# Kernel optimization log

Measured on AMD Instinct MI355X. Metric: run time of the kernel, lower is better.

Reference implementation:

```python
import jax, jax.numpy as jnp
import numpy as np

B, HEAD, IMG, STRIDE, C = 8, 512, 1280, 32, 20
FMP = IMG // STRIDE            # 40
N = FMP * FMP                  # 1600 grid cells
CONF_T, NMS_T = 0.001, 0.6


def setup_inputs() -> dict:
    key = jax.random.key(0)
    ks = jax.random.split(key, 8)
    s3 = 1.0 / np.sqrt(HEAD * 9)   # fan-in scaled 3x3 weights
    s1 = 1.0 / np.sqrt(HEAD)
    return {
        "x": jax.random.normal(ks[0], (B, HEAD, FMP, FMP), jnp.float32),
        "cls_w": jax.random.normal(ks[1], (2, HEAD, HEAD, 3, 3), jnp.float32) * s3,
        "cls_b": jnp.zeros((2, HEAD), jnp.float32),
        "reg_w": jax.random.normal(ks[2], (4, HEAD, HEAD, 3, 3), jnp.float32) * s3,
        "reg_b": jnp.zeros((4, HEAD), jnp.float32),
        "obj_w": jax.random.normal(ks[3], (1, HEAD, 1, 1), jnp.float32) * s1,
        "obj_b": jnp.zeros((1,), jnp.float32),
        "clsp_w": jax.random.normal(ks[4], (C, HEAD, 1, 1), jnp.float32) * s1,
        "clsp_b": jnp.zeros((C,), jnp.float32),
        "regp_w": jax.random.normal(ks[5], (4, HEAD, 1, 1), jnp.float32) * s1,
        "regp_b": jnp.zeros((4,), jnp.float32),
    }


def _conv(x, w, b, pad):
    y = jax.lax.conv_general_dilated(
        x, w, (1, 1), [(pad, pad), (pad, pad)],
        dimension_numbers=("NCHW", "OIHW", "NCHW"))
    return y + b[None, :, None, None]


def _leaky(v):
    return jnp.where(v > 0, v, 0.1 * v)


def _head(x, cls_w, cls_b, reg_w, reg_b, obj_w, obj_b, clsp_w, clsp_b, regp_w, regp_b):
    cf = x
    for i in range(2):
        cf = _leaky(_conv(cf, cls_w[i], cls_b[i], 1))
    rf = x
    for i in range(4):
        rf = _leaky(_conv(rf, reg_w[i], reg_b[i], 1))
    b = x.shape[0]
    obj = _conv(rf, obj_w, obj_b, 0).reshape(b, 1, N).transpose(0, 2, 1)   # [B,N,1]
    cls = _conv(cf, clsp_w, clsp_b, 0).reshape(b, C, N).transpose(0, 2, 1) # [B,N,C]
    reg = _conv(rf, regp_w, regp_b, 0).reshape(b, 4, N).transpose(0, 2, 1) # [B,N,4]
    # decode_bbox (center_sample=False)
    gy, gx = jnp.meshgrid(jnp.arange(FMP), jnp.arange(FMP), indexing="ij")
    grid = jnp.stack([gx, gy], -1).reshape(N, 2).astype(jnp.float32)       # [N,2]
    xy = jax.nn.sigmoid(reg[..., :2]) + grid
    wh = jnp.exp(reg[..., 2:])
    box = jnp.concatenate([xy - wh * 0.5, xy + wh * 0.5], -1) * STRIDE     # [B,N,4]
    bboxes = jnp.clip(box / IMG, 0.0, 1.0)
    scores = jax.nn.sigmoid(obj) * jax.nn.softmax(cls, axis=-1)            # [B,N,C]
    return bboxes, scores


def _nms_mask(iou, scores, mask):
    # greedy NMS over boxes where mask is True; returns bool keep mask [N]
    order = jnp.argsort(-jnp.where(mask, scores, -jnp.inf))
    rank = jnp.argsort(order)  # rank[j] = position of box j in score order
    def body(i, keep):
        idx = order[i]
        sup = (iou[idx] > NMS_T) & keep[idx] & (rank > i)
        return keep & ~sup
    return jax.lax.fori_loop(0, scores.shape[0], body, mask)


def _post_one(boxes, scores):
    # boxes [N,4], scores [N,C] -> per-image postprocess
    cls_inds = jnp.argmax(scores, axis=1)
    best = jnp.take_along_axis(scores, cls_inds[:, None], axis=1)[:, 0]
    conf = best >= CONF_T
    x1, y1, x2, y2 = boxes[:, 0], boxes[:, 1], boxes[:, 2], boxes[:, 3]
    areas = (x2 - x1) * (y2 - y1)
    xx1 = jnp.maximum(x1[:, None], x1[None, :])
    yy1 = jnp.maximum(y1[:, None], y1[None, :])
    xx2 = jnp.minimum(x2[:, None], x2[None, :])
    yy2 = jnp.minimum(y2[:, None], y2[None, :])
    w = jnp.maximum(1e-28, xx2 - xx1)
    h = jnp.maximum(1e-28, yy2 - yy1)
    inter = w * h
    iou = inter / (areas[:, None] + areas[None, :] - inter + 1e-14)  # [N,N]
    keep_c = jax.vmap(
        lambda c: _nms_mask(iou, best, conf & (cls_inds == c)))(jnp.arange(C))
    return best, cls_inds.astype(jnp.int32), keep_c.any(0)


def reference(x, cls_w, cls_b, reg_w, reg_b, obj_w, obj_b,
              clsp_w, clsp_b, regp_w, regp_b):
    bboxes, scores = _head(x, cls_w, cls_b, reg_w, reg_b,
                           obj_w, obj_b, clsp_w, clsp_b, regp_w, regp_b)
    best, cls_inds, keep = jax.vmap(_post_one)(bboxes, scores)
    # fixed-shape outputs: boxes [B,N,4], best score [B,N], class id [B,N], keep mask [B,N]
    return bboxes, best, cls_inds, keep
```

## Files before the change

### kernel.cpp

```cpp
#include <hip/hip_runtime.h>
#include <math.h>

#define CH    512
#define FMPX  40
#define PW    42
#define PADN  1764
#define NP    1600
#define BATCH 8
#define NCLS  20
#define CONF_THR 0.001f
#define NMS_THR  0.6f

typedef _Float16 v8h __attribute__((ext_vector_type(8)));
typedef float    v4f __attribute__((ext_vector_type(4)));

#define FPLANE  ((size_t)BATCH * PADN * CH)
#define WSZ     ((size_t)9 * CH * CH)

__device__ __forceinline__ int padidx(int p) { return p + 2 * (p / FMPX) + PW + 1; }

typedef __attribute__((address_space(1))) const void* gas_t;
typedef __attribute__((address_space(3))) void*       las_t;
__device__ __forceinline__ void gl2lds16(const void* g, void* l) {
    __builtin_amdgcn_global_load_lds((gas_t)g, (las_t)l, 16, 0, 0);
}
__device__ __forceinline__ unsigned lds_addr(void* p) {
    return (unsigned)(uintptr_t)(las_t)p;
}
__device__ __forceinline__ v8h lds_b128(unsigned a) {
    v8h r;
    asm volatile("ds_read_b128 %0, %1" : "=v"(r) : "v"(a));
    return r;
}

__global__ __launch_bounds__(256)
void border_zero(uint4* __restrict__ ws) {
    int idx = blockIdx.x * 256 + threadIdx.x;
    int u    = idx & 63;
    int cell = (idx >> 6) % 164;
    int b    = (idx / (64 * 164)) & 7;
    int pl   = idx / (64 * 164 * 8);
    int pi;
    if (cell < 42)      pi = cell;
    else if (cell < 84) pi = 41 * PW + (cell - 42);
    else { int r = cell - 84; pi = (1 + (r >> 1)) * PW + ((r & 1) ? 41 : 0); }
    size_t hoff = (size_t)pl * FPLANE + (size_t)b * (PADN * CH) + (size_t)pi * CH;
    ws[(hoff >> 3) + u] = make_uint4(0u, 0u, 0u, 0u);
}

__global__ __launch_bounds__(256)
void xprep_kernel(const float* __restrict__ x, _Float16* __restrict__ Xh,
                  _Float16* __restrict__ Xl) {
    __shared__ float T[64][65];
    const int t = threadIdx.x;
    const int p0  = blockIdx.x * 64;
    const int ci0 = blockIdx.y * 64;
    const int b   = blockIdx.z;
#pragma unroll
    for (int it = 0; it < 16; ++it) {
        int row = (t >> 6) + 4 * it;
        int col = t & 63;
        T[col][row] = x[((size_t)b * CH + ci0 + row) * NP + p0 + col];
    }
    __syncthreads();
#pragma unroll
    for (int it = 0; it < 16; ++it) {
        int posl = (t >> 6) + 4 * it;
        int ci   = t & 63;
        float v = T[posl][ci];
        _Float16 h = (_Float16)v;
        _Float16 l = (_Float16)((v - (float)h) * 2048.0f);
        size_t o = (size_t)b * (PADN * CH) + (size_t)padidx(p0 + posl) * CH + ci0 + ci;
        Xh[o] = h; Xl[o] = l;
    }
}

__global__ __launch_bounds__(256)
void wtrans_kernel(const float* __restrict__ w, _Float16* __restrict__ Wh,
                   _Float16* __restrict__ Wl) {
    __shared__ float tile[32][289];
    const int t = threadIdx.x;
    const int co0 = blockIdx.x * 32;
    const int ci0 = blockIdx.y * 32;
#pragma unroll
    for (int g = 0; g < 36; ++g) {
        int l = t + 256 * g;
        int co = l / 288, j = l - co * 288;
        tile[co][j] = w[(size_t)(co0 + co) * 4608 + ci0 * 9 + j];
    }
    __syncthreads();
#pragma unroll
    for (int tap = 0; tap < 9; ++tap) {
#pragma unroll
        for (int cg = 0; cg < 4; ++cg) {
            int co = cg * 8 + (t >> 5);
            int ci = t & 31;
            float v = tile[co][ci * 9 + tap];
            _Float16 h = (_Float16)(16.0f * v);
            _Float16 l = (_Float16)((v - (float)h * 0.0625f) * 32768.0f);
            size_t o = ((size_t)tap * CH + co0 + co) * CH + ci0 + ci;
            Wh[o] = h; Wl[o] = l;
        }
    }
}

__global__ __launch_bounds__(512, 2)
void conv_dual(const _Float16* __restrict__ I0h, const _Float16* __restrict__ I0l,
               const _Float16* __restrict__ W0h, const _Float16* __restrict__ W0l,
               const float* __restrict__ bias0,
               _Float16* __restrict__ O0h, _Float16* __restrict__ O0l,
               const _Float16* __restrict__ I1h, const _Float16* __restrict__ I1l,
               const _Float16* __restrict__ W1h, const _Float16* __restrict__ W1l,
               const float* __restrict__ bias1,
               _Float16* __restrict__ O1h, _Float16* __restrict__ O1l) {
    __shared__ _Float16 sm[73728];
    const int t = threadIdx.x;
    const int w = t >> 6, l = t & 63;
    const int quad = l >> 4, col = l & 15;
    const int ph = w >> 2, cq = w & 3;

    const int bid = blockIdx.x;
    const int b   = bid & 7;
    const int q   = bid >> 3;
    const int cid = q / 26;
    const int r   = q - 26 * cid;
    const int co0 = (r & 1) * 256;
    const int p0  = (r >> 1) * 128;

    const _Float16* Ih = cid ? I1h : I0h;
    const _Float16* Il = cid ? I1l : I0l;
    const _Float16* Wh = cid ? W1h : W0h;
    const _Float16* Wl = cid ? W1l : W0l;
    const float*  bias = cid ? bias1 : bias0;
    _Float16* Oh = cid ? O1h : O0h;
    _Float16* Ol = cid ? O1l : O0l;

    const size_t boff = (size_t)b * (PADN * CH);

    const size_t sA  = boff + (size_t)padidx(p0 + 16 * w + col) * CH + quad * 8;
    const size_t sB0 = (size_t)(co0 + 32 * w + col) * CH + quad * 8;
    const int dA = w * 512 + l * 8;
    const int dB = 8192 + (2 * w) * 512 + l * 8;

    const unsigned smB = lds_addr(sm);
    unsigned aRh[4], aRl[4], bRh[4], bRl[4];
#pragma unroll
    for (int i = 0; i < 4; ++i) {
        aRh[i] = smB + (ph * 4 + i) * 1024 + l * 16;
        aRl[i] = aRh[i] + 8192;
    }
#pragma unroll
    for (int j = 0; j < 4; ++j) {
        bRh[j] = smB + 16384 + (cq * 4 + j) * 1024 + l * 16;
        bRl[j] = bRh[j] + 16384;
    }

    auto stage_chunk = [&](int mm, unsigned nH) {
        const int tap = mm >> 4, cc = (mm & 15) << 5;
        const int ty  = tap / 3;
        const int tsh = ((ty - 1) * PW + (tap - ty * 3 - 1)) * CH + cc;
        const size_t wo = (size_t)tap * (CH * CH) + cc;
        gl2lds16(Ih + sA + tsh,           sm + nH + dA);
        gl2lds16(Il + sA + tsh,           sm + nH + 4096 + dA);
        gl2lds16(Wh + wo + sB0,           sm + nH + dB);
        gl2lds16(Wh + wo + sB0 + 16 * CH, sm + nH + dB + 512);
        gl2lds16(Wl + wo + sB0,           sm + nH + 8192 + dB);
        gl2lds16(Wl + wo + sB0 + 16 * CH, sm + nH + 8192 + dB + 512);
    };

    v4f acc1[4][4], acc2[4][4];
#pragma unroll
    for (int i = 0; i < 4; ++i)
#pragma unroll
        for (int j = 0; j < 4; ++j) {
            acc1[i][j] = (v4f){0.f, 0.f, 0.f, 0.f};
            acc2[i][j] = (v4f){0.f, 0.f, 0.f, 0.f};
        }

    stage_chunk(0, 0);
    stage_chunk(1, 24576);
    asm volatile("s_waitcnt vmcnt(6)" ::: "memory");
    __builtin_amdgcn_s_barrier();

    unsigned c0H = 0, c1H = 24576, c2H = 49152;

#pragma unroll 1
    for (int m = 0; m < 144; ++m) {
        const unsigned bufB = c0H * 2;

        v8h ah[4], al[4], bh[4], bl[4];
#pragma unroll
        for (int i = 0; i < 4; ++i) {
            ah[i] = lds_b128(aRh[i] + bufB);
            al[i] = lds_b128(aRl[i] + bufB);
        }
        bh[0] = lds_b128(bRh[0] + bufB);
        bl[0] = lds_b128(bRl[0] + bufB);

        if (m < 142) stage_chunk(m + 2, c2H);

#pragma unroll
        for (int j = 0; j < 4; ++j) {
            if (j < 3) {
                bh[j + 1] = lds_b128(bRh[j + 1] + bufB);
                bl[j + 1] = lds_b128(bRl[j + 1] + bufB);
                asm volatile("s_waitcnt lgkmcnt(2)" ::: "memory");
            } else {
                asm volatile("s_waitcnt lgkmcnt(0)" ::: "memory");
            }
            __builtin_amdgcn_sched_barrier(0);
            __builtin_amdgcn_s_setprio(1);
#pragma unroll
            for (int i = 0; i < 4; ++i)
                acc1[i][j] = __builtin_amdgcn_mfma_f32_16x16x32_f16(ah[i], bh[j], acc1[i][j], 0, 0, 0);
#pragma unroll
            for (int i = 0; i < 4; ++i)
                acc2[i][j] = __builtin_amdgcn_mfma_f32_16x16x32_f16(ah[i], bl[j], acc2[i][j], 0, 0, 0);
#pragma unroll
            for (int i = 0; i < 4; ++i)
                acc2[i][j] = __builtin_amdgcn_mfma_f32_16x16x32_f16(al[i], bh[j], acc2[i][j], 0, 0, 0);
            __builtin_amdgcn_s_setprio(0);
        }

        if (m < 142) {
            asm volatile("s_waitcnt vmcnt(6)" ::: "memory");
            __builtin_amdgcn_s_barrier();
        } else if (m == 142) {
            asm volatile("s_waitcnt vmcnt(0)" ::: "memory");
            __builtin_amdgcn_s_barrier();
        }
        unsigned tmp = c0H; c0H = c1H; c1H = c2H; c2H = tmp;
    }

#pragma unroll
    for (int i = 0; i < 4; ++i) {
#pragma unroll
        for (int j = 0; j < 4; ++j) {
            int n = co0 + cq * 64 + j * 16 + col;
            float bv = bias[n];
#pragma unroll
            for (int rr = 0; rr < 4; ++rr) {
                int p = p0 + ph * 64 + i * 16 + quad * 4 + rr;
                if (p < NP) {
                    float v = acc1[i][j][rr] * 0.0625f + acc2[i][j][rr] * (1.0f / 32768.0f) + bv;
                    v = v > 0.f ? v : 0.1f * v;
                    _Float16 h = (_Float16)v;
                    _Float16 lo = (_Float16)((v - (float)h) * 2048.0f);
                    size_t o = boff + (size_t)padidx(p) * CH + n;
                    Oh[o] = h; Ol[o] = lo;
                }
            }
        }
    }
}

__global__ __launch_bounds__(256)
void head_kernel(const _Float16* __restrict__ Rh, const _Float16* __restrict__ Rl,
                 const _Float16* __restrict__ Ch, const _Float16* __restrict__ Cl,
                 const float* __restrict__ objw, const float* __restrict__ objb,
                 const float* __restrict__ clsw, const float* __restrict__ clsb,
                 const float* __restrict__ regw, const float* __restrict__ regb,
                 float* __restrict__ out) {
    const int wid = (blockIdx.x * 256 + threadIdx.x) >> 6;
    const int l = threadIdx.x & 63;
    const int b = wid / NP, p = wid - b * NP;
    const size_t base = (size_t)b * (PADN * CH) + (size_t)padidx(p) * CH + l * 8;

    v8h rh = *(const v8h*)(Rh + base), rl = *(const v8h*)(Rl + base);
    v8h ch = *(const v8h*)(Ch + base), cl = *(const v8h*)(Cl + base);
    float rv[8], cv[8];
#pragma unroll
    for (int k = 0; k < 8; ++k) {
        rv[k] = (float)rh[k] + (float)rl[k] * (1.0f / 2048.0f);
        cv[k] = (float)ch[k] + (float)cl[k] * (1.0f / 2048.0f);
    }
    float s[25];
#pragma unroll
    for (int o = 0; o < 25; ++o) s[o] = 0.f;
#pragma unroll
    for (int k = 0; k < 8; ++k) s[0] = fmaf(objw[l * 8 + k], rv[k], s[0]);
#pragma unroll
    for (int c = 0; c < NCLS; ++c)
#pragma unroll
        for (int k = 0; k < 8; ++k) s[1 + c] = fmaf(clsw[c * CH + l * 8 + k], cv[k], s[1 + c]);
#pragma unroll
    for (int q = 0; q < 4; ++q)
#pragma unroll
        for (int k = 0; k < 8; ++k) s[21 + q] = fmaf(regw[q * CH + l * 8 + k], rv[k], s[21 + q]);
#pragma unroll
    for (int o = 0; o < 25; ++o) {
#pragma unroll
        for (int off = 32; off > 0; off >>= 1) s[o] += __shfl_xor(s[o], off);
    }
    if (l == 0) {
        int gp = b * NP + p;
        float obj  = s[0] + objb[0];
        float sobj = 1.f / (1.f + expf(-obj));
        float lg[NCLS];
        float m = -1e30f; int am = 0;
#pragma unroll
        for (int c = 0; c < NCLS; ++c) {
            lg[c] = s[1 + c] + clsb[c];
            if (lg[c] > m) { m = lg[c]; am = c; }
        }
        float se = 0.f;
#pragma unroll
        for (int c = 0; c < NCLS; ++c) se += expf(lg[c] - m);
        float best = sobj / se;

        float r0 = s[21] + regb[0], r1 = s[22] + regb[1];
        float r2 = s[23] + regb[2], r3 = s[24] + regb[3];
        int gy = p / FMPX, gx = p - gy * FMPX;
        float cx = 1.f / (1.f + expf(-r0)) + (float)gx;
        float cy = 1.f / (1.f + expf(-r1)) + (float)gy;
        float hw = 0.5f * expf(r2);
        float hh = 0.5f * expf(r3);
        const float sc = 32.f / 1280.f;
        float x1 = fminf(fmaxf((cx - hw) * sc, 0.f), 1.f);
        float y1 = fminf(fmaxf((cy - hh) * sc, 0.f), 1.f);
        float x2 = fminf(fmaxf((cx + hw) * sc, 0.f), 1.f);
        float y2 = fminf(fmaxf((cy + hh) * sc, 0.f), 1.f);

        ((float4*)out)[gp] = make_float4(x1, y1, x2, y2);
        out[4 * BATCH * NP + gp] = best;
        out[5 * BATCH * NP + gp] = (float)am;
        out[6 * BATCH * NP + gp] = 0.f;
    }
}

__global__ __launch_bounds__(1024)
void nms_kernel(float* __restrict__ out) {
    const int c = blockIdx.x, b = blockIdx.y;
    const int t = threadIdx.x;
    const int w = t >> 6, l = t & 63;

    __shared__ unsigned long long skey[2048];
    __shared__ float4 CBox[NP];
    __shared__ float4 KBox[1664];
    __shared__ unsigned long long wmask[16];
    __shared__ int Kcnt;

    for (int j = t; j < NP; j += 1024) {
        int gp = b * NP + j;
        float4 bx = ((const float4*)out)[gp];
        float best = out[4 * BATCH * NP + gp];
        int   ci   = (int)out[5 * BATCH * NP + gp];
        CBox[j] = bx;
        bool alive = (ci == c) && (best >= CONF_THR);
        unsigned long long key = alive
            ? ~(((unsigned long long)__float_as_uint(best) << 32)
                | (unsigned long long)(0xFFFFFFFFu - (unsigned)j))
            : ~0ull;
        skey[j] = key;
    }
    for (int j = NP + t; j < 2048; j += 1024) skey[j] = ~0ull;
    for (int j = t; j < 1664; j += 1024) KBox[j] = make_float4(0.f, 0.f, 0.f, 0.f);
    if (t == 0) Kcnt = 0;

    for (unsigned k = 2; k <= 2048; k <<= 1) {
        for (unsigned j = k >> 1; j > 0; j >>= 1) {
            __syncthreads();
            for (unsigned i = t; i < 2048; i += 1024) {
                unsigned p = i ^ j;
                if (p > i) {
                    bool up = ((i & k) == 0);
                    unsigned long long a = skey[i], bq = skey[p];
                    if ((a > bq) == up) { skey[i] = bq; skey[p] = a; }
                }
            }
        }
    }
    __syncthreads();

    float* keepout = out + 6 * BATCH * NP + b * NP;
    for (int base = 0; base < NP; base += 64) {
        unsigned long long ik = skey[base + l];
        bool valid = (ik != ~0ull);
        unsigned long long vm = __ballot(valid);
        if (vm == 0) break;

        unsigned idx = 0;
        float4 bx = make_float4(0.f, 0.f, 0.f, 0.f);
        float ar = 0.f;
        if (valid) {
            unsigned long long K = ~ik;
            idx = 0xFFFFFFFFu - (unsigned)(K & 0xFFFFFFFFull);
            bx  = CBox[idx];
            ar  = (bx.z - bx.x) * (bx.w - bx.y);
        }
        int prevK = Kcnt;
        int prevKpad = (prevK + 63) & ~63;

        bool sup = false;
        for (int kk = w * 4; kk < prevKpad; kk += 64) {
            float4 kb0 = KBox[kk],     kb1 = KBox[kk + 1];
            float4 kb2 = KBox[kk + 2], kb3 = KBox[kk + 3];
#pragma unroll
            for (int q = 0; q < 4; ++q) {
                float4 kb = q == 0 ? kb0 : q == 1 ? kb1 : q == 2 ? kb2 : kb3;
                float kar = (kb.z - kb.x) * (kb.w - kb.y);
                float xx1 = fmaxf(kb.x, bx.x);
                float yy1 = fmaxf(kb.y, bx.y);
                float xx2 = fminf(kb.z, bx.z);
                float yy2 = fminf(kb.w, bx.w);
                float ww = fmaxf(1e-28f, xx2 - xx1);
                float hh = fmaxf(1e-28f, yy2 - yy1);
                float inter = ww * hh;
                float iou = inter / (kar + ar - inter + 1e-14f);
                sup |= (iou > NMS_THR);
            }
        }
        wmask[w] = __ballot(valid && !sup);
        __syncthreads();

        if (w == 0) {
            unsigned long long alive = wmask[0];
#pragma unroll
            for (int q = 1; q < 16; ++q) alive &= wmask[q];
            unsigned long long smask = 0;
            for (int s = 0; s < 63; ++s) {
                float ox1 = __shfl(bx.x, s), oy1 = __shfl(bx.y, s);
                float ox2 = __shfl(bx.z, s), oy2 = __shfl(bx.w, s);
                float oar = (ox2 - ox1) * (oy2 - oy1);
                float xx1 = fmaxf(ox1, bx.x);
                float yy1 = fmaxf(oy1, bx.y);
                float xx2 = fminf(ox2, bx.z);
                float yy2 = fminf(oy2, bx.w);
                float ww = fmaxf(1e-28f, xx2 - xx1);
                float hh = fmaxf(1e-28f, yy2 - yy1);
                float inter = ww * hh;
                float iou = inter / (oar + ar - inter + 1e-14f);
                if (s < l && iou > NMS_THR) smask |= (1ull << s);
            }
            unsigned long long kept = 0;
            while (alive) {
                int s = __builtin_ctzll(alive);
                kept |= (1ull << s);
                alive &= ~(1ull << s);
                unsigned long long dead = __ballot((smask >> s) & 1ull);
                alive &= ~dead;
            }
            if ((kept >> l) & 1ull) {
                int pos = prevK + __builtin_popcountll(kept & ((1ull << l) - 1ull));
                KBox[pos] = bx;
                keepout[idx] = 1.0f;
            }
            if (l == 0) Kcnt = prevK + __builtin_popcountll(kept);
        }
        __syncthreads();
    }
}

extern "C" void kernel_launch(void* const* d_in, const int* in_sizes, int n_in,
                              void* d_out, int out_size, void* d_ws, size_t ws_size,
                              hipStream_t stream) {
    const float* x      = (const float*)d_in[0];
    const float* cls_w  = (const float*)d_in[1];
    const float* cls_b  = (const float*)d_in[2];
    const float* reg_w  = (const float*)d_in[3];
    const float* reg_b  = (const float*)d_in[4];
    const float* obj_w  = (const float*)d_in[5];
    const float* obj_b  = (const float*)d_in[6];
    const float* clsp_w = (const float*)d_in[7];
    const float* clsp_b = (const float*)d_in[8];
    const float* regp_w = (const float*)d_in[9];
    const float* regp_b = (const float*)d_in[10];
    float* out = (float*)d_out;

    _Float16* ws = (_Float16*)d_ws;
    _Float16* Xh = ws;
    _Float16* Xl = ws + FPLANE;
    _Float16* Ah = ws + 2 * FPLANE;
    _Float16* Al = ws + 3 * FPLANE;
    _Float16* Bh = ws + 4 * FPLANE;
    _Float16* Bl = ws + 5 * FPLANE;
    _Float16* Ch = ws + 6 * FPLANE;
    _Float16* Cl = ws + 7 * FPLANE;
    _Float16* W0h = ws + 8 * FPLANE;
    _Float16* W0l = W0h + WSZ;
    _Float16* W1h = W0l + WSZ;
    _Float16* W1l = W1h + WSZ;
    const size_t LW = (size_t)CH * CH * 9;

    border_zero<<<dim3(2624), 256, 0, stream>>>((uint4*)d_ws);
    xprep_kernel<<<dim3(25, 8, 8), 256, 0, stream>>>(x, Xh, Xl);

    dim3 wgrid(16, 16), blk(256);

    wtrans_kernel<<<wgrid, blk, 0, stream>>>(cls_w, W0h, W0l);
    wtrans_kernel<<<wgrid, blk, 0, stream>>>(reg_w, W1h, W1l);
    conv_dual<<<dim3(416), 512, 0, stream>>>(Xh, Xl, W0h, W0l, cls_b,      Ah, Al,
                                             Xh, Xl, W1h, W1l, reg_b,      Ch, Cl);
    wtrans_kernel<<<wgrid, blk, 0, stream>>>(cls_w + LW, W0h, W0l);
    wtrans_kernel<<<wgrid, blk, 0, stream>>>(reg_w + LW, W1h, W1l);
    conv_dual<<<dim3(416), 512, 0, stream>>>(Ah, Al, W0h, W0l, cls_b + CH, Bh, Bl,
                                             Ch, Cl, W1h, W1l, reg_b + CH, Xh, Xl);
    wtrans_kernel<<<wgrid, blk, 0, stream>>>(reg_w + 2 * LW, W0h, W0l);
    conv_dual<<<dim3(208), 512, 0, stream>>>(Xh, Xl, W0h, W0l, reg_b + 2 * CH, Ch, Cl,
                                             Xh, Xl, W0h, W0l, reg_b + 2 * CH, Ch, Cl);
    wtrans_kernel<<<wgrid, blk, 0, stream>>>(reg_w + 3 * LW, W0h, W0l);
    conv_dual<<<dim3(208), 512, 0, stream>>>(Ch, Cl, W0h, W0l, reg_b + 3 * CH, Xh, Xl,
                                             Ch, Cl, W0h, W0l, reg_b + 3 * CH, Xh, Xl);

    head_kernel<<<dim3(3200), 256, 0, stream>>>(Xh, Xl, Bh, Bl, obj_w, obj_b,
                                                clsp_w, clsp_b, regp_w, regp_b, out);
    nms_kernel<<<dim3(NCLS, BATCH), 1024, 0, stream>>>(out);
}
```

Measured before the change: 1.735 ms.

## Load activation fragments directly from global into registers, stage only weights in LDS

The conv kernel stops staging the activation (A) hi/lo tiles through LDS. Each wave now loads its A fragments straight from global memory into registers, double-buffered across an unrolled pair of iterations, and only the weight hi/lo tiles go through the triple-buffered LDS ring. This shrinks LDS use and removes the LDS write/read traffic for activations. It also reorders the MFMAs so the hi-hi products run before the weight-lo fragments are read. The cost is redundant global loads: waves that share a row tile each fetch the same activations, with more register pressure and longer global latency exposed inside the loop.

Result: slower. 2.882 ms (+66.1%).

```diff
diff --git a/kernel.cpp b/kernel.cpp
--- a/kernel.cpp
+++ b/kernel.cpp
@@ -113,7 +113,7 @@
                const _Float16* __restrict__ W1h, const _Float16* __restrict__ W1l,
                const float* __restrict__ bias1,
                _Float16* __restrict__ O1h, _Float16* __restrict__ O1l) {
-    __shared__ _Float16 sm[73728];
+    __shared__ _Float16 sm[49152];
     const int t = threadIdx.x;
     const int w = t >> 6, l = t & 63;
     const int quad = l >> 4, col = l & 15;
@@ -128,7 +128,6 @@
     const int p0  = (r >> 1) * 128;
 
     const _Float16* Ih = cid ? I1h : I0h;
-    const _Float16* Il = cid ? I1l : I0l;
     const _Float16* Wh = cid ? W1h : W0h;
     const _Float16* Wl = cid ? W1l : W0l;
     const float*  bias = cid ? bias1 : bias0;
@@ -137,35 +136,41 @@
 
     const size_t boff = (size_t)b * (PADN * CH);
 
-    const size_t sA  = boff + (size_t)padidx(p0 + 16 * w + col) * CH + quad * 8;
     const size_t sB0 = (size_t)(co0 + 32 * w + col) * CH + quad * 8;
-    const int dA = w * 512 + l * 8;
-    const int dB = 8192 + (2 * w) * 512 + l * 8;
+    const int dB = (2 * w) * 512 + l * 8;
 
     const unsigned smB = lds_addr(sm);
-    unsigned aRh[4], aRl[4], bRh[4], bRl[4];
-#pragma unroll
-    for (int i = 0; i < 4; ++i) {
-        aRh[i] = smB + (ph * 4 + i) * 1024 + l * 16;
-        aRl[i] = aRh[i] + 8192;
-    }
+    unsigned bRh[4], bRl[4];
 #pragma unroll
     for (int j = 0; j < 4; ++j) {
-        bRh[j] = smB + 16384 + (cq * 4 + j) * 1024 + l * 16;
+        bRh[j] = smB + (cq * 4 + j) * 1024 + l * 16;
         bRl[j] = bRh[j] + 16384;
     }
 
-    auto stage_chunk = [&](int mm, unsigned nH) {
-        const int tap = mm >> 4, cc = (mm & 15) << 5;
+    unsigned sAw[4];
+#pragma unroll
+    for (int i = 0; i < 4; ++i)
+        sAw[i] = (unsigned)(boff + (size_t)padidx(p0 + (ph * 4 + i) * 16 + col) * CH + quad * 8);
+
+    const _Float16 *pA0, *pA1, *pA2, *pA3, *pWh, *pWl;
+    auto setA = [&](int ms) {
+        const int tap = ms >> 4, cc = (ms & 15) << 5;
         const int ty  = tap / 3;
         const int tsh = ((ty - 1) * PW + (tap - ty * 3 - 1)) * CH + cc;
+        pA0 = Ih + sAw[0] + tsh;  pA1 = Ih + sAw[1] + tsh;
+        pA2 = Ih + sAw[2] + tsh;  pA3 = Ih + sAw[3] + tsh;
+    };
+    auto setW = [&](int ms) {
+        const int tap = ms >> 4, cc = (ms & 15) << 5;
         const size_t wo = (size_t)tap * (CH * CH) + cc;
-        gl2lds16(Ih + sA + tsh,           sm + nH + dA);
-        gl2lds16(Il + sA + tsh,           sm + nH + 4096 + dA);
-        gl2lds16(Wh + wo + sB0,           sm + nH + dB);
-        gl2lds16(Wh + wo + sB0 + 16 * CH, sm + nH + dB + 512);
-        gl2lds16(Wl + wo + sB0,           sm + nH + 8192 + dB);
-        gl2lds16(Wl + wo + sB0 + 16 * CH, sm + nH + 8192 + dB + 512);
+        pWh = Wh + wo + sB0;  pWl = Wl + wo + sB0;
+    };
+    auto stageB = [&](unsigned byteOff) {
+        _Float16* dst = (_Float16*)((char*)sm + byteOff) + dB;
+        gl2lds16(pWh,           dst);
+        gl2lds16(pWh + 16 * CH, dst + 512);
+        gl2lds16(pWl,           dst + 8192);
+        gl2lds16(pWl + 16 * CH, dst + 8192 + 512);
     };
 
     v4f acc1[4][4], acc2[4][4];
@@ -177,59 +182,99 @@
             acc2[i][j] = (v4f){0.f, 0.f, 0.f, 0.f};
         }
 
-    stage_chunk(0, 0);
-    stage_chunk(1, 24576);
-    asm volatile("s_waitcnt vmcnt(6)" ::: "memory");
+    unsigned c0B = 0, c1B = 32768, c2B = 65536;
+
+    v8h ahP[4], ahQ[4];
+    setA(0);
+    ahP[0] = *(const v8h*)pA0;  ahP[1] = *(const v8h*)pA1;
+    ahP[2] = *(const v8h*)pA2;  ahP[3] = *(const v8h*)pA3;
+    setW(0); stageB(0);
+    setW(1); stageB(32768);
+    setW(2);
+    asm volatile("s_waitcnt vmcnt(4)" ::: "memory");
     __builtin_amdgcn_s_barrier();
 
-    unsigned c0H = 0, c1H = 24576, c2H = 49152;
-
-#pragma unroll 1
-    for (int m = 0; m < 144; ++m) {
-        const unsigned bufB = c0H * 2;
-
-        v8h ah[4], al[4], bh[4], bl[4];
-#pragma unroll
-        for (int i = 0; i < 4; ++i) {
-            ah[i] = lds_b128(aRh[i] + bufB);
-            al[i] = lds_b128(aRl[i] + bufB);
-        }
-        bh[0] = lds_b128(bRh[0] + bufB);
-        bl[0] = lds_b128(bRl[0] + bufB);
-
-        if (m < 142) stage_chunk(m + 2, c2H);
-
-#pragma unroll
-        for (int j = 0; j < 4; ++j) {
-            if (j < 3) {
-                bh[j + 1] = lds_b128(bRh[j + 1] + bufB);
-                bl[j + 1] = lds_b128(bRl[j + 1] + bufB);
-                asm volatile("s_waitcnt lgkmcnt(2)" ::: "memory");
-            } else {
-                asm volatile("s_waitcnt lgkmcnt(0)" ::: "memory");
-            }
-            __builtin_amdgcn_sched_barrier(0);
-            __builtin_amdgcn_s_setprio(1);
-#pragma unroll
-            for (int i = 0; i < 4; ++i)
-                acc1[i][j] = __builtin_amdgcn_mfma_f32_16x16x32_f16(ah[i], bh[j], acc1[i][j], 0, 0, 0);
+    auto chunk_body = [&](int m, v8h (&ah)[4], v8h (&ahN)[4]) {
+        const unsigned rb = c0B;
+
+        v8h bh[4];
+        bh[0] = lds_b128(bRh[0] + rb);
+        bh[1] = lds_b128(bRh[1] + rb);
+        bh[2] = lds_b128(bRh[2] + rb);
+        bh[3] = lds_b128(bRh[3] + rb);
+
+        v8h al[4];
+        al[0] = *(const v8h*)(pA0 + FPLANE);
+        al[1] = *(const v8h*)(pA1 + FPLANE);
+        al[2] = *(const v8h*)(pA2 + FPLANE);
+        al[3] = *(const v8h*)(pA3 + FPLANE);
+
+        if (m < 143) { asm volatile("s_waitcnt vmcnt(8) lgkmcnt(0)" ::: "memory"); }
+        else         { asm volatile("s_waitcnt vmcnt(4) lgkmcnt(0)" ::: "memory"); }
+        __builtin_amdgcn_sched_barrier(0);
+
+        __builtin_amdgcn_s_setprio(1);
+#pragma unroll
+        for (int i = 0; i < 4; ++i)
+            acc1[i][0] = __builtin_amdgcn_mfma_f32_16x16x32_f16(ah[i], bh[0], acc1[i][0], 0, 0, 0);
+#pragma unroll
+        for (int i = 0; i < 4; ++i)
+            acc1[i][1] = __builtin_amdgcn_mfma_f32_16x16x32_f16(ah[i], bh[1], acc1[i][1], 0, 0, 0);
+#pragma unroll
+        for (int i = 0; i < 4; ++i)
+            acc1[i][2] = __builtin_amdgcn_mfma_f32_16x16x32_f16(ah[i], bh[2], acc1[i][2], 0, 0, 0);
+#pragma unroll
+        for (int i = 0; i < 4; ++i)
+            acc1[i][3] = __builtin_amdgcn_mfma_f32_16x16x32_f16(ah[i], bh[3], acc1[i][3], 0, 0, 0);
+        __builtin_amdgcn_s_setprio(0);
+
+        v8h bl[4];
+        bl[0] = lds_b128(bRl[0] + rb);
+        bl[1] = lds_b128(bRl[1] + rb);
+        bl[2] = lds_b128(bRl[2] + rb);
+        bl[3] = lds_b128(bRl[3] + rb);
+
+        if (m < 143) {
+            if (((m + 1) & 15) == 0) setA(m + 1);
+            else { pA0 += 32; pA1 += 32; pA2 += 32; pA3 += 32; }
+            ahN[0] = *(const v8h*)pA0;  ahN[1] = *(const v8h*)pA1;
+            ahN[2] = *(const v8h*)pA2;  ahN[3] = *(const v8h*)pA3;
+        }
+        if (m < 142) {
+            stageB(c2B);
+            const int nx = m + 3;
+            if (nx < 144) {
+                if ((nx & 15) == 0) setW(nx);
+                else { pWh += 32; pWl += 32; }
+            }
+        }
+
+        if (m < 142)       { asm volatile("s_waitcnt vmcnt(8) lgkmcnt(0)" ::: "memory"); }
+        else if (m == 142) { asm volatile("s_waitcnt vmcnt(4) lgkmcnt(0)" ::: "memory"); }
+        else               { asm volatile("s_waitcnt vmcnt(0) lgkmcnt(0)" ::: "memory"); }
+        __builtin_amdgcn_sched_barrier(0);
+
+        __builtin_amdgcn_s_setprio(1);
+#pragma unroll
+        for (int j = 0; j < 4; ++j)
 #pragma unroll
             for (int i = 0; i < 4; ++i)
                 acc2[i][j] = __builtin_amdgcn_mfma_f32_16x16x32_f16(ah[i], bl[j], acc2[i][j], 0, 0, 0);
 #pragma unroll
+        for (int j = 0; j < 4; ++j)
+#pragma unroll
             for (int i = 0; i < 4; ++i)
                 acc2[i][j] = __builtin_amdgcn_mfma_f32_16x16x32_f16(al[i], bh[j], acc2[i][j], 0, 0, 0);
-            __builtin_amdgcn_s_setprio(0);
-        }
-
-        if (m < 142) {
-            asm volatile("s_waitcnt vmcnt(6)" ::: "memory");
-            __builtin_amdgcn_s_barrier();
-        } else if (m == 142) {
-            asm volatile("s_waitcnt vmcnt(0)" ::: "memory");
-            __builtin_amdgcn_s_barrier();
-        }
-        unsigned tmp = c0H; c0H = c1H; c1H = c2H; c2H = tmp;
+        __builtin_amdgcn_s_setprio(0);
+
+        if (m < 143) __builtin_amdgcn_s_barrier();
+        unsigned tmp = c0B; c0B = c1B; c1B = c2B; c2B = tmp;
+    };
+
+#pragma unroll 1
+    for (int mo = 0; mo < 144; mo += 2) {
+        chunk_body(mo,     ahP, ahQ);
+        chunk_body(mo + 1, ahQ, ahP);
     }
 
 #pragma unroll
```
